# Performance work log

Measured on AMD Instinct MI355X. Metric: run time of the kernel, lower is better.

## Reference

```python
import jax, jax.numpy as jnp
import numpy as np

B, T, E, H = 2, 4096, 768, 12
D = E // H  # head_dim = 64


def setup_inputs() -> dict:
    key = jax.random.key(0)
    ks = jax.random.split(key, 9)
    s = 1.0 / np.sqrt(E)
    return {
        "x": jax.random.normal(ks[0], (B, T, E), dtype=jnp.float32),
        "wq": jax.random.normal(ks[1], (E, E), dtype=jnp.float32) * s,
        "bq": jnp.zeros((E,), dtype=jnp.float32),
        "wk": jax.random.normal(ks[2], (E, E), dtype=jnp.float32) * s,
        "bk": jnp.zeros((E,), dtype=jnp.float32),
        "wv": jax.random.normal(ks[3], (E, E), dtype=jnp.float32) * s,
        "bv": jnp.zeros((E,), dtype=jnp.float32),
        "wo": jax.random.normal(ks[4], (E, E), dtype=jnp.float32) * s,
        "bo": jnp.zeros((E,), dtype=jnp.float32),
    }


def reference(x, wq, bq, wk, bk, wv, bv, wo, bo):
    # Linear projections (torch Linear: x @ W.T + b; weights here stored as (in,out))
    q = x @ wq + bq  # (B,T,E)
    k = x @ wk + bk
    v = x @ wv + bv

    def split(t):
        return t.reshape(B, T, H, D).transpose(0, 2, 1, 3)  # (B,H,T,D)

    q, k, v = split(q), split(k), split(v)
    scale = 1.0 / np.sqrt(D).astype(np.float32)
    scores = jnp.einsum("bhtd,bhsd->bhts", q, k) * scale  # (B,H,T,T)
    causal = jnp.tril(jnp.ones((T, T), dtype=bool))
    scores = jnp.where(causal, scores, -jnp.inf)
    attn = jax.nn.softmax(scores, axis=-1)
    out = jnp.einsum("bhts,bhsd->bhtd", attn, v)  # (B,H,T,D)
    out = out.transpose(0, 2, 1, 3).reshape(B, T, E)
    return out @ wo + bo
```

## Files before the change

kernel.cpp:

```cpp
#include <hip/hip_runtime.h>
#include <hip/hip_bf16.h>

#define TSEQ 4096
#define EMB 768
#define NH 12
#define DH 64
#define BT 8192
#define NROWS (24 * TSEQ)

typedef __attribute__((ext_vector_type(8))) short bf16x8;
typedef __attribute__((ext_vector_type(4))) float f32x4;

#define FENCE() asm volatile("" ::: "memory")

__device__ __forceinline__ f32x4 mfma16(bf16x8 a, bf16x8 b, f32x4 c) {
    return __builtin_amdgcn_mfma_f32_16x16x32_bf16(a, b, c, 0, 0, 0);
}

__device__ __forceinline__ void gload16(const void* g, void* l) {
    __builtin_amdgcn_global_load_lds((const __attribute__((address_space(1))) void*)g,
                                     (__attribute__((address_space(3))) void*)l, 16, 0, 0);
}

__device__ __forceinline__ float bf2f(unsigned short u) {
    return __uint_as_float(((unsigned)u) << 16);
}

__global__ __launch_bounds__(256) void conv_all_k(const float* __restrict__ x,
                                                  __hip_bfloat16* __restrict__ xb,
                                                  const float* w0, const float* w1,
                                                  const float* w2, const float* w3,
                                                  __hip_bfloat16* o0, __hip_bfloat16* o1,
                                                  __hip_bfloat16* o2, __hip_bfloat16* o3) {
    __shared__ float tile[32][33];
    int bid = blockIdx.x;
    if (bid < 6144) {
        int i = (bid * 256 + threadIdx.x) * 4;
        float4 v = *(const float4*)(x + i);
        union { unsigned short u[4]; uint2 p; } o;
        __hip_bfloat16 t0 = __float2bfloat16(v.x); o.u[0] = *(unsigned short*)&t0;
        __hip_bfloat16 t1 = __float2bfloat16(v.y); o.u[1] = *(unsigned short*)&t1;
        __hip_bfloat16 t2 = __float2bfloat16(v.z); o.u[2] = *(unsigned short*)&t2;
        __hip_bfloat16 t3 = __float2bfloat16(v.w); o.u[3] = *(unsigned short*)&t3;
        *(uint2*)(xb + i) = o.p;
        return;
    }
    bid -= 6144;
    const int z = bid / 576, rr = bid % 576, by = rr / 24, bx = rr % 24;
    const float* w; __hip_bfloat16* o;
    switch (z) {
        case 0: w = w0; o = o0; break;
        case 1: w = w1; o = o1; break;
        case 2: w = w2; o = o2; break;
        default: w = w3; o = o3; break;
    }
    int tx = threadIdx.x & 31, ty = threadIdx.x >> 5;
    int kb = by * 32, nb = bx * 32;
    for (int i = 0; i < 32; i += 8)
        tile[ty + i][tx] = w[(size_t)(kb + ty + i) * EMB + nb + tx];
    __syncthreads();
    for (int i = 0; i < 32; i += 8)
        o[(size_t)(nb + ty + i) * EMB + kb + tx] = __float2bfloat16(tile[tx][ty + i]);
}

__device__ __forceinline__ void gemm_body(const __hip_bfloat16* __restrict__ A,
                                          const __hip_bfloat16* __restrict__ Wt,
                                          const float* __restrict__ bias,
                                          void* __restrict__ outp, int mode, float scale) {
    __shared__ alignas(16) char As[2][8192];
    __shared__ alignas(16) char Bs[2][8192];
    const int m0 = blockIdx.x * 128, n0 = blockIdx.y * 128;
    const int tid = threadIdx.x;
    const int lane = tid & 63, l15 = lane & 15, lg = lane >> 4;
    const int wave = tid >> 6, wm = wave >> 1, wn = wave & 1;
    const int swz = (l15 & 7) << 4;

    int mrow_[2]; int kelem_[2];
#pragma unroll
    for (int c = 0; c < 2; ++c) {
        int p = c * 4096 + tid * 16;
        int lrow = p >> 7, w = p & 127;
        int wp = w ^ ((lrow & 7) << 4);
        mrow_[c] = lrow + ((wp >> 6) & 1) * 64;
        kelem_[c] = (wp & 63) >> 1;
    }

    f32x4 acc[4][4];
    for (int i = 0; i < 4; ++i)
        for (int j = 0; j < 4; ++j) acc[i][j] = (f32x4){0.f, 0.f, 0.f, 0.f};

    auto stage = [&](int buf, int k0) {
#pragma unroll
        for (int c = 0; c < 2; ++c)
            gload16(A + (size_t)(m0 + mrow_[c]) * EMB + k0 + kelem_[c],
                    As[buf] + c * 4096 + wave * 1024);
#pragma unroll
        for (int c = 0; c < 2; ++c)
            gload16(Wt + (size_t)(n0 + mrow_[c]) * EMB + k0 + kelem_[c],
                    Bs[buf] + c * 4096 + wave * 1024);
    };

    stage(0, 0);
    const int NK = EMB / 32;
    for (int ks = 0; ks < NK; ++ks) {
        const int cur = ks & 1;
        asm volatile("s_waitcnt vmcnt(0)" ::: "memory");
        FENCE(); __builtin_amdgcn_s_barrier(); FENCE();
        if (ks + 1 < NK) stage(cur ^ 1, (ks + 1) * 32);
        bf16x8 af[4], bfv[4];
#pragma unroll
        for (int f = 0; f < 4; ++f)
            af[f] = *(const bf16x8*)(As[cur] + (f * 16 + l15) * 128 + ((wm * 64 + lg * 16) ^ swz));
#pragma unroll
        for (int f = 0; f < 4; ++f)
            bfv[f] = *(const bf16x8*)(Bs[cur] + (f * 16 + l15) * 128 + ((wn * 64 + lg * 16) ^ swz));
        __builtin_amdgcn_s_setprio(1);
#pragma unroll
        for (int i = 0; i < 4; ++i)
#pragma unroll
            for (int j = 0; j < 4; ++j)
                acc[i][j] = mfma16(af[i], bfv[j], acc[i][j]);
        __builtin_amdgcn_s_setprio(0);
    }

#pragma unroll
    for (int i = 0; i < 4; ++i) {
#pragma unroll
        for (int j = 0; j < 4; ++j) {
            const int n = n0 + wn * 64 + j * 16 + l15;
            const float bv = bias[n];
            const int mbase = m0 + wm * 64 + i * 16 + lg * 4;
#pragma unroll
            for (int r = 0; r < 4; ++r) {
                const int m = mbase + r;
                const float val = (acc[i][j][r] + bv) * scale;
                if (mode == 2) {
                    ((float*)outp)[(size_t)m * EMB + n] = val;
                } else {
                    const int b = m >> 12, t = m & (TSEQ - 1);
                    const int h = n >> 6, d = n & 63;
                    size_t addr;
                    if (mode == 0) addr = ((size_t)(b * NH + h) * TSEQ + t) * DH + d;
                    else           addr = ((size_t)(b * NH + h) * DH + d) * TSEQ + t;
                    ((__hip_bfloat16*)outp)[addr] = __float2bfloat16(val);
                }
            }
        }
    }
}

__global__ __launch_bounds__(256) void qkv_k(const __hip_bfloat16* __restrict__ xb,
                                             const __hip_bfloat16* __restrict__ wqT,
                                             const __hip_bfloat16* __restrict__ wkT,
                                             const __hip_bfloat16* __restrict__ wvT,
                                             const float* __restrict__ bq,
                                             const float* __restrict__ bk,
                                             const float* __restrict__ bv,
                                             __hip_bfloat16* __restrict__ qo,
                                             __hip_bfloat16* __restrict__ ko,
                                             __hip_bfloat16* __restrict__ vo) {
    const __hip_bfloat16* Wt; const float* bias; void* o; int mode; float scale;
    const float cq = 0.125f * 1.44269504089f;
    switch (blockIdx.z) {
        case 0:  Wt = wqT; bias = bq; o = qo; mode = 0; scale = cq;  break;
        case 1:  Wt = wkT; bias = bk; o = ko; mode = 0; scale = 1.f; break;
        default: Wt = wvT; bias = bv; o = vo; mode = 1; scale = 1.f; break;
    }
    gemm_body(xb, Wt, bias, o, mode, scale);
}

__global__ __launch_bounds__(256) void oprojc_k(const __hip_bfloat16* __restrict__ opart,
                                                const float* __restrict__ lpart,
                                                const __hip_bfloat16* __restrict__ Wt,
                                                const float* __restrict__ bias,
                                                float* __restrict__ out) {
    __shared__ alignas(16) char As[2][4096];
    __shared__ alignas(16) char Bs[2][8192];
    const int m0 = blockIdx.x * 64, n0 = blockIdx.y * 128;
    const int tid = threadIdx.x;
    const int lane = tid & 63, l15 = lane & 15, lg = lane >> 4;
    const int wave = tid >> 6, wm = wave >> 1, wn = wave & 1;
    const int swz = (l15 & 7) << 4;

    int amrow, akelem;
    {
        int p = tid * 16;
        int lrow = p >> 7, w = p & 127;
        int wp = w ^ ((lrow & 7) << 4);
        amrow = lrow + ((wp >> 6) & 1) * 32;
        akelem = (wp & 63) >> 1;
    }
    const int m = m0 + amrow;
    const int b_ = m >> 12, t = m & (TSEQ - 1);
    int bnrow[2], bkelem[2];
#pragma unroll
    for (int c = 0; c < 2; ++c) {
        int p = c * 4096 + tid * 16;
        int lrow = p >> 7, w = p & 127;
        int wp = w ^ ((lrow & 7) << 4);
        bnrow[c] = lrow + ((wp >> 6) & 1) * 64;
        bkelem[c] = (wp & 63) >> 1;
    }

    f32x4 acc[2][4];
    for (int i = 0; i < 2; ++i)
        for (int j = 0; j < 4; ++j) acc[i][j] = (f32x4){0.f, 0.f, 0.f, 0.f};

    auto stage = [&](int buf, int k0) {
        const int h = k0 >> 6;
        const int d0 = (k0 & 63) + akelem;
        const size_t orow = ((size_t)(b_ * NH + h)) * TSEQ + t;
        bf16x8 a0 = *(const bf16x8*)(opart + orow * DH + d0);
        bf16x8 a1 = *(const bf16x8*)(opart + ((size_t)NROWS + orow) * DH + d0);
        const float li = 1.0f / (lpart[orow] + lpart[NROWS + orow]);
        union { unsigned w[4]; uint4 v; } pk;
#pragma unroll
        for (int jp = 0; jp < 4; ++jp) {
            const float e0 = (bf2f((unsigned short)a0[2 * jp]) + bf2f((unsigned short)a1[2 * jp])) * li;
            const float e1 = (bf2f((unsigned short)a0[2 * jp + 1]) + bf2f((unsigned short)a1[2 * jp + 1])) * li;
            asm("v_cvt_pk_bf16_f32 %0, %1, %2" : "=v"(pk.w[jp]) : "v"(e0), "v"(e1));
        }
        *(uint4*)(As[buf] + wave * 1024 + lane * 16) = pk.v;
#pragma unroll
        for (int c = 0; c < 2; ++c)
            gload16(Wt + (size_t)(n0 + bnrow[c]) * EMB + k0 + bkelem[c],
                    Bs[buf] + c * 4096 + wave * 1024);
    };

    stage(0, 0);
    const int NK = EMB / 32;
    for (int ks = 0; ks < NK; ++ks) {
        const int cur = ks & 1;
        asm volatile("s_waitcnt vmcnt(0) lgkmcnt(0)" ::: "memory");
        FENCE(); __builtin_amdgcn_s_barrier(); FENCE();
        if (ks + 1 < NK) stage(cur ^ 1, (ks + 1) * 32);
        bf16x8 af[2], bfv[4];
#pragma unroll
        for (int f = 0; f < 2; ++f)
            af[f] = *(const bf16x8*)(As[cur] + (f * 16 + l15) * 128 + ((wm * 64 + lg * 16) ^ swz));
#pragma unroll
        for (int f = 0; f < 4; ++f)
            bfv[f] = *(const bf16x8*)(Bs[cur] + (f * 16 + l15) * 128 + ((wn * 64 + lg * 16) ^ swz));
        __builtin_amdgcn_s_setprio(1);
#pragma unroll
        for (int i = 0; i < 2; ++i)
#pragma unroll
            for (int j = 0; j < 4; ++j)
                acc[i][j] = mfma16(af[i], bfv[j], acc[i][j]);
        __builtin_amdgcn_s_setprio(0);
    }

#pragma unroll
    for (int i = 0; i < 2; ++i) {
#pragma unroll
        for (int j = 0; j < 4; ++j) {
            const int n = n0 + wn * 64 + j * 16 + l15;
            const float bv = bias[n];
            const int mbase = m0 + wm * 32 + i * 16 + lg * 4;
#pragma unroll
            for (int r = 0; r < 4; ++r)
                out[(size_t)(mbase + r) * EMB + n] = acc[i][j][r] + bv;
        }
    }
}

__global__ __launch_bounds__(256, 3) void attn_k(const __hip_bfloat16* __restrict__ qb,
                                                 const __hip_bfloat16* __restrict__ kb,
                                                 const __hip_bfloat16* __restrict__ vt,
                                                 __hip_bfloat16* __restrict__ opart,
                                                 float* __restrict__ lpart) {
    __shared__ alignas(16) char Ks[8192];
    __shared__ alignas(16) char Vs[8192];
    __shared__ alignas(16) char pbuf[4][4096];
    const int lane = threadIdx.x & 63, l15 = lane & 15, lg = lane >> 4;
    const int wave = threadIdx.x >> 6;
    const int bid = blockIdx.x;
    const int xcd = bid & 7, slot = bid >> 3;
    const int pair = slot & 31;
    const int parity = (slot >> 5) & 1;
    const int hgrp = slot >> 6;
    const int bh = xcd + hgrp * 8;
    const __hip_bfloat16* Qh = qb + (size_t)bh * TSEQ * DH;
    const __hip_bfloat16* Kh = kb + (size_t)bh * TSEQ * DH;
    const __hip_bfloat16* Vh = vt + (size_t)bh * DH * TSEQ;
    char* Pb = pbuf[wave];
    const int swz = (l15 & 7) << 4;
    const float M0 = 12.0f;

    bf16x8 ones8;
#pragma unroll
    for (int j = 0; j < 8; ++j) ones8[j] = (short)0x3F80;

    unsigned ka[8];
#pragma unroll
    for (int st = 0; st < 4; ++st)
#pragma unroll
        for (int ks = 0; ks < 2; ++ks)
            ka[st * 2 + ks] = (unsigned)((st * 16 + l15) * 128 + ((ks * 64 + lg * 16) ^ swz));
    char* pwh[4]; char* prh[2]; char* pwl[4]; char* prl[2];
#pragma unroll
    for (int st = 0; st < 4; ++st) {
        pwh[st] = Pb + l15 * 128 + ((st * 32 + lg * 8) ^ swz);
        pwl[st] = pwh[st] + 2048;
    }
#pragma unroll
    for (int ks = 0; ks < 2; ++ks) {
        prh[ks] = Pb + l15 * 128 + ((ks * 64 + lg * 16) ^ swz);
        prl[ks] = prh[ks] + 2048;
    }
    const int dthr = wave * 16 + l15 - lg * 4;

    int r_[2], wp_[2];
#pragma unroll
    for (int c = 0; c < 2; ++c) {
        int p = c * 4096 + wave * 1024 + lane * 16;
        int r = p >> 7, w = p & 127;
        r_[c] = r;
        wp_[c] = (w ^ ((r & 7) << 4)) >> 1;
    }

    const int lo = pair, hi = 63 - pair;
    const int q0l = lo * 64 + wave * 16;
    const int q0h = hi * 64 + wave * 16;
    const int nsb = hi + 1;

    bf16x8 qh0 = *(const bf16x8*)(Qh + (size_t)(q0h + l15) * DH + lg * 8);
    bf16x8 qh1 = *(const bf16x8*)(Qh + (size_t)(q0h + l15) * DH + 32 + lg * 8);
    bf16x8 ql0 = *(const bf16x8*)(Qh + (size_t)(q0l + l15) * DH + lg * 8);
    bf16x8 ql1 = *(const bf16x8*)(Qh + (size_t)(q0l + l15) * DH + 32 + lg * 8);

    f32x4 oh[4], ol[4];
#pragma unroll
    for (int dt = 0; dt < 4; ++dt) { oh[dt] = (f32x4){0.f,0.f,0.f,0.f}; ol[dt] = (f32x4){0.f,0.f,0.f,0.f}; }
    f32x4 lh = (f32x4){0.f,0.f,0.f,0.f}, ll = (f32x4){0.f,0.f,0.f,0.f};

    const char* kg0 = (const char*)(Kh + (size_t)r_[0] * DH + wp_[0]) + parity * 8192;
    const char* kg1 = (const char*)(Kh + (size_t)r_[1] * DH + wp_[1]) + parity * 8192;
    const char* vg0 = (const char*)(Vh + (size_t)r_[0] * TSEQ + wp_[0]) + parity * 128;
    const char* vg1 = (const char*)(Vh + (size_t)r_[1] * TSEQ + wp_[1]) + parity * 128;

#define STAGE() do {                                                             \
    gload16(kg0, Ks + wave * 1024);                                              \
    gload16(kg1, Ks + 4096 + wave * 1024);                                       \
    gload16(vg0, Vs + wave * 1024);                                              \
    gload16(vg1, Vs + 4096 + wave * 1024);                                       \
    kg0 += 16384; kg1 += 16384; vg0 += 256; vg1 += 256;                          \
} while (0)

#define QKSM(KF, Q0, Q1, MASKB, PW) do {                                         \
    f32x4 sa[4];                                                                 \
    __builtin_amdgcn_s_setprio(1);                                               \
    _Pragma("unroll")                                                            \
    for (int st = 0; st < 4; ++st) {                                             \
        f32x4 z = (f32x4){0.f, 0.f, 0.f, 0.f};                                   \
        z = mfma16(KF[st * 2 + 0], Q0, z);                                       \
        z = mfma16(KF[st * 2 + 1], Q1, z);                                       \
        sa[st] = z;                                                              \
    }                                                                            \
    __builtin_amdgcn_s_setprio(0);                                               \
    if (MASKB) {                                                                 \
        _Pragma("unroll")                                                        \
        for (int st = 0; st < 4; ++st)                                           \
            _Pragma("unroll")                                                    \
            for (int r = 0; r < 4; ++r)                                          \
                if (st * 16 + r > dthr) sa[st][r] = -INFINITY;                   \
    }                                                                            \
    _Pragma("unroll")                                                            \
    for (int st = 0; st < 4; ++st) {                                             \
        const float e0 = exp2f(sa[st][0] - M0);                                  \
        const float e1 = exp2f(sa[st][1] - M0);                                  \
        const float e2 = exp2f(sa[st][2] - M0);                                  \
        const float e3 = exp2f(sa[st][3] - M0);                                  \
        uint2 pkv;                                                               \
        asm("v_cvt_pk_bf16_f32 %0, %1, %2" : "=v"(pkv.x) : "v"(e0), "v"(e1));    \
        asm("v_cvt_pk_bf16_f32 %0, %1, %2" : "=v"(pkv.y) : "v"(e2), "v"(e3));    \
        *(uint2*)PW[st] = pkv;                                                   \
    }                                                                            \
} while (0)

#define PVU(VF, OV, LA, PR) do {                                                 \
    bf16x8 pf0 = *(const bf16x8*)PR[0];                                          \
    bf16x8 pf1 = *(const bf16x8*)PR[1];                                          \
    __builtin_amdgcn_s_setprio(1);                                               \
    LA = mfma16(pf0, ones8, LA);                                                 \
    LA = mfma16(pf1, ones8, LA);                                                 \
    _Pragma("unroll")                                                            \
    for (int dt = 0; dt < 4; ++dt)                                               \
        OV[dt] = mfma16(pf0, VF[dt * 2 + 0], OV[dt]);                            \
    _Pragma("unroll")                                                            \
    for (int dt = 0; dt < 4; ++dt)                                               \
        OV[dt] = mfma16(pf1, VF[dt * 2 + 1], OV[dt]);                            \
    __builtin_amdgcn_s_setprio(0);                                               \
} while (0)

    STAGE();
    for (int sb = parity; sb < nsb; sb += 2) {
        const bool loact = (sb <= lo);
        asm volatile("s_waitcnt vmcnt(0)" ::: "memory");
        FENCE(); __builtin_amdgcn_s_barrier(); FENCE();
        bf16x8 kf[8];
#pragma unroll
        for (int i = 0; i < 8; ++i) kf[i] = *(const bf16x8*)(Ks + ka[i]);
        QKSM(kf, qh0, qh1, (sb == hi), pwh);
        if (loact) QKSM(kf, ql0, ql1, (sb == lo), pwl);
        bf16x8 vf[8];
#pragma unroll
        for (int i = 0; i < 8; ++i) vf[i] = *(const bf16x8*)(Vs + ka[i]);
        asm volatile("s_waitcnt lgkmcnt(0)" ::: "memory");
        FENCE(); __builtin_amdgcn_s_barrier(); FENCE();
        if (sb + 2 < nsb) STAGE();
        PVU(vf, oh, lh, prh);
        if (loact) PVU(vf, ol, ll, prl);
    }

#undef PVU
#undef QKSM
#undef STAGE

    const size_t prow = ((size_t)parity * 24 + bh) * TSEQ;
    {
#pragma unroll
        for (int r = 0; r < 4; ++r) {
            const size_t base = (prow + q0h + lg * 4 + r) * DH;
#pragma unroll
            for (int dt = 0; dt < 4; ++dt)
                opart[base + dt * 16 + l15] = __float2bfloat16(oh[dt][r]);
        }
        if (l15 == 0) {
#pragma unroll
            for (int r = 0; r < 4; ++r) lpart[prow + q0h + lg * 4 + r] = lh[r];
        }
    }
    {
#pragma unroll
        for (int r = 0; r < 4; ++r) {
            const size_t base = (prow + q0l + lg * 4 + r) * DH;
#pragma unroll
            for (int dt = 0; dt < 4; ++dt)
                opart[base + dt * 16 + l15] = __float2bfloat16(ol[dt][r]);
        }
        if (l15 == 0) {
#pragma unroll
            for (int r = 0; r < 4; ++r) lpart[prow + q0l + lg * 4 + r] = ll[r];
        }
    }
}

extern "C" void kernel_launch(void* const* d_in, const int* in_sizes, int n_in,
                              void* d_out, int out_size, void* d_ws, size_t ws_size,
                              hipStream_t stream) {
    (void)in_sizes; (void)n_in; (void)out_size; (void)ws_size;
    const float* x  = (const float*)d_in[0];
    const float* wq = (const float*)d_in[1];
    const float* bq = (const float*)d_in[2];
    const float* wk = (const float*)d_in[3];
    const float* bk = (const float*)d_in[4];
    const float* wv = (const float*)d_in[5];
    const float* bv = (const float*)d_in[6];
    const float* wo = (const float*)d_in[7];
    const float* bo = (const float*)d_in[8];
    float* out = (float*)d_out;

    char* ws = (char*)d_ws;
    size_t off = 0;
    auto alloc = [&](size_t bytes) {
        char* p = ws + off;
        off += (bytes + 255) & ~(size_t)255;
        return p;
    };
    __hip_bfloat16* xb   = (__hip_bfloat16*)alloc((size_t)BT * EMB * 2);
    __hip_bfloat16* qbf  = (__hip_bfloat16*)alloc((size_t)BT * EMB * 2);
    __hip_bfloat16* kbf  = (__hip_bfloat16*)alloc((size_t)BT * EMB * 2);
    __hip_bfloat16* vtb  = (__hip_bfloat16*)alloc((size_t)BT * EMB * 2);
    __hip_bfloat16* wqT  = (__hip_bfloat16*)alloc((size_t)EMB * EMB * 2);
    __hip_bfloat16* wkT  = (__hip_bfloat16*)alloc((size_t)EMB * EMB * 2);
    __hip_bfloat16* wvT  = (__hip_bfloat16*)alloc((size_t)EMB * EMB * 2);
    __hip_bfloat16* woT  = (__hip_bfloat16*)alloc((size_t)EMB * EMB * 2);
    __hip_bfloat16* opart = (__hip_bfloat16*)alloc((size_t)2 * NROWS * DH * 2);
    float*          lpart = (float*)alloc((size_t)2 * NROWS * 4);

    conv_all_k<<<6144 + 2304, 256, 0, stream>>>(x, xb, wq, wk, wv, wo, wqT, wkT, wvT, woT);
    qkv_k<<<dim3(64, 6, 3), 256, 0, stream>>>(xb, wqT, wkT, wvT, bq, bk, bv, qbf, kbf, vtb);
    attn_k<<<1536, 256, 0, stream>>>(qbf, kbf, vtb, opart, lpart);
    oprojc_k<<<dim3(128, 6), 256, 0, stream>>>(opart, lpart, woT, bo, out);
}
```

Before: 183.7 us.

## Split hi/lo query tiles across separate waves in 512-thread attention blocks

The attention kernel now uses 8 waves per block instead of 4. Waves 0-3 handle the high query tile and waves 4-7 the low tile, where before each wave processed both tiles in sequence. Each thread stages half as many K/V loads, and each wave's P buffer shrinks to 2KB. This is meant to raise parallelism and cut per-wave register pressure. The cost is that the low-tile waves sit idle, only hitting barriers, once past their causal limit, and there are more waves per block to synchronise.

```diff
diff --git a/kernel.cpp b/kernel.cpp
--- a/kernel.cpp
+++ b/kernel.cpp
@@ -264,16 +264,19 @@
     }
 }
 
-__global__ __launch_bounds__(256, 3) void attn_k(const __hip_bfloat16* __restrict__ qb,
+__global__ __launch_bounds__(512, 4) void attn_k(const __hip_bfloat16* __restrict__ qb,
                                                  const __hip_bfloat16* __restrict__ kb,
                                                  const __hip_bfloat16* __restrict__ vt,
                                                  __hip_bfloat16* __restrict__ opart,
                                                  float* __restrict__ lpart) {
     __shared__ alignas(16) char Ks[8192];
     __shared__ alignas(16) char Vs[8192];
-    __shared__ alignas(16) char pbuf[4][4096];
-    const int lane = threadIdx.x & 63, l15 = lane & 15, lg = lane >> 4;
-    const int wave = threadIdx.x >> 6;
+    __shared__ alignas(16) char pbuf[8][2048];
+    const int tid = threadIdx.x;
+    const int lane = tid & 63, l15 = lane & 15, lg = lane >> 4;
+    const int wave = tid >> 6;
+    const int w4 = wave & 3;
+    const bool hirole = (wave < 4);
     const int bid = blockIdx.x;
     const int xcd = bid & 7, slot = bid >> 3;
     const int pair = slot & 31;
@@ -297,64 +300,51 @@
 #pragma unroll
         for (int ks = 0; ks < 2; ++ks)
             ka[st * 2 + ks] = (unsigned)((st * 16 + l15) * 128 + ((ks * 64 + lg * 16) ^ swz));
-    char* pwh[4]; char* prh[2]; char* pwl[4]; char* prl[2];
-#pragma unroll
-    for (int st = 0; st < 4; ++st) {
-        pwh[st] = Pb + l15 * 128 + ((st * 32 + lg * 8) ^ swz);
-        pwl[st] = pwh[st] + 2048;
-    }
-#pragma unroll
-    for (int ks = 0; ks < 2; ++ks) {
-        prh[ks] = Pb + l15 * 128 + ((ks * 64 + lg * 16) ^ swz);
-        prl[ks] = prh[ks] + 2048;
-    }
-    const int dthr = wave * 16 + l15 - lg * 4;
-
-    int r_[2], wp_[2];
-#pragma unroll
-    for (int c = 0; c < 2; ++c) {
-        int p = c * 4096 + wave * 1024 + lane * 16;
+    char* pw[4]; char* pr[2];
+#pragma unroll
+    for (int st = 0; st < 4; ++st) pw[st] = Pb + l15 * 128 + ((st * 32 + lg * 8) ^ swz);
+#pragma unroll
+    for (int ks = 0; ks < 2; ++ks) pr[ks] = Pb + l15 * 128 + ((ks * 64 + lg * 16) ^ swz);
+    const int dthr = w4 * 16 + l15 - lg * 4;
+
+    int r_, wp_;
+    {
+        int p = tid * 16;
         int r = p >> 7, w = p & 127;
-        r_[c] = r;
-        wp_[c] = (w ^ ((r & 7) << 4)) >> 1;
+        r_ = r;
+        wp_ = (w ^ ((r & 7) << 4)) >> 1;
     }
 
     const int lo = pair, hi = 63 - pair;
-    const int q0l = lo * 64 + wave * 16;
-    const int q0h = hi * 64 + wave * 16;
+    const int mytile = hirole ? hi : lo;
+    const int q0 = mytile * 64 + w4 * 16;
     const int nsb = hi + 1;
 
-    bf16x8 qh0 = *(const bf16x8*)(Qh + (size_t)(q0h + l15) * DH + lg * 8);
-    bf16x8 qh1 = *(const bf16x8*)(Qh + (size_t)(q0h + l15) * DH + 32 + lg * 8);
-    bf16x8 ql0 = *(const bf16x8*)(Qh + (size_t)(q0l + l15) * DH + lg * 8);
-    bf16x8 ql1 = *(const bf16x8*)(Qh + (size_t)(q0l + l15) * DH + 32 + lg * 8);
-
-    f32x4 oh[4], ol[4];
-#pragma unroll
-    for (int dt = 0; dt < 4; ++dt) { oh[dt] = (f32x4){0.f,0.f,0.f,0.f}; ol[dt] = (f32x4){0.f,0.f,0.f,0.f}; }
-    f32x4 lh = (f32x4){0.f,0.f,0.f,0.f}, ll = (f32x4){0.f,0.f,0.f,0.f};
-
-    const char* kg0 = (const char*)(Kh + (size_t)r_[0] * DH + wp_[0]) + parity * 8192;
-    const char* kg1 = (const char*)(Kh + (size_t)r_[1] * DH + wp_[1]) + parity * 8192;
-    const char* vg0 = (const char*)(Vh + (size_t)r_[0] * TSEQ + wp_[0]) + parity * 128;
-    const char* vg1 = (const char*)(Vh + (size_t)r_[1] * TSEQ + wp_[1]) + parity * 128;
+    bf16x8 q0f = *(const bf16x8*)(Qh + (size_t)(q0 + l15) * DH + lg * 8);
+    bf16x8 q1f = *(const bf16x8*)(Qh + (size_t)(q0 + l15) * DH + 32 + lg * 8);
+
+    f32x4 ov[4];
+#pragma unroll
+    for (int dt = 0; dt < 4; ++dt) ov[dt] = (f32x4){0.f, 0.f, 0.f, 0.f};
+    f32x4 la = (f32x4){0.f, 0.f, 0.f, 0.f};
+
+    const char* kg = (const char*)(Kh + (size_t)r_ * DH + wp_) + parity * 8192;
+    const char* vg = (const char*)(Vh + (size_t)r_ * TSEQ + wp_) + parity * 128;
 
 #define STAGE() do {                                                             \
-    gload16(kg0, Ks + wave * 1024);                                              \
-    gload16(kg1, Ks + 4096 + wave * 1024);                                       \
-    gload16(vg0, Vs + wave * 1024);                                              \
-    gload16(vg1, Vs + 4096 + wave * 1024);                                       \
-    kg0 += 16384; kg1 += 16384; vg0 += 256; vg1 += 256;                          \
+    gload16(kg, Ks + wave * 1024);                                               \
+    gload16(vg, Vs + wave * 1024);                                               \
+    kg += 16384; vg += 256;                                                      \
 } while (0)
 
-#define QKSM(KF, Q0, Q1, MASKB, PW) do {                                         \
+#define QKSM(KF, MASKB) do {                                                     \
     f32x4 sa[4];                                                                 \
     __builtin_amdgcn_s_setprio(1);                                               \
     _Pragma("unroll")                                                            \
     for (int st = 0; st < 4; ++st) {                                             \
         f32x4 z = (f32x4){0.f, 0.f, 0.f, 0.f};                                   \
-        z = mfma16(KF[st * 2 + 0], Q0, z);                                       \
-        z = mfma16(KF[st * 2 + 1], Q1, z);                                       \
+        z = mfma16(KF[st * 2 + 0], q0f, z);                                      \
+        z = mfma16(KF[st * 2 + 1], q1f, z);                                      \
         sa[st] = z;                                                              \
     }                                                                            \
     __builtin_amdgcn_s_setprio(0);                                               \
@@ -374,43 +364,47 @@
         uint2 pkv;                                                               \
         asm("v_cvt_pk_bf16_f32 %0, %1, %2" : "=v"(pkv.x) : "v"(e0), "v"(e1));    \
         asm("v_cvt_pk_bf16_f32 %0, %1, %2" : "=v"(pkv.y) : "v"(e2), "v"(e3));    \
-        *(uint2*)PW[st] = pkv;                                                   \
+        *(uint2*)pw[st] = pkv;                                                   \
     }                                                                            \
 } while (0)
 
-#define PVU(VF, OV, LA, PR) do {                                                 \
-    bf16x8 pf0 = *(const bf16x8*)PR[0];                                          \
-    bf16x8 pf1 = *(const bf16x8*)PR[1];                                          \
+#define PVU(VF) do {                                                             \
+    bf16x8 pf0 = *(const bf16x8*)pr[0];                                          \
+    bf16x8 pf1 = *(const bf16x8*)pr[1];                                          \
     __builtin_amdgcn_s_setprio(1);                                               \
-    LA = mfma16(pf0, ones8, LA);                                                 \
-    LA = mfma16(pf1, ones8, LA);                                                 \
+    la = mfma16(pf0, ones8, la);                                                 \
+    la = mfma16(pf1, ones8, la);                                                 \
     _Pragma("unroll")                                                            \
     for (int dt = 0; dt < 4; ++dt)                                               \
-        OV[dt] = mfma16(pf0, VF[dt * 2 + 0], OV[dt]);                            \
+        ov[dt] = mfma16(pf0, VF[dt * 2 + 0], ov[dt]);                            \
     _Pragma("unroll")                                                            \
     for (int dt = 0; dt < 4; ++dt)                                               \
-        OV[dt] = mfma16(pf1, VF[dt * 2 + 1], OV[dt]);                            \
+        ov[dt] = mfma16(pf1, VF[dt * 2 + 1], ov[dt]);                            \
     __builtin_amdgcn_s_setprio(0);                                               \
 } while (0)
 
     STAGE();
     for (int sb = parity; sb < nsb; sb += 2) {
-        const bool loact = (sb <= lo);
+        const bool act = hirole || (sb <= lo);
+        const bool maskb = hirole ? (sb == hi) : (sb == lo);
         asm volatile("s_waitcnt vmcnt(0)" ::: "memory");
         FENCE(); __builtin_amdgcn_s_barrier(); FENCE();
-        bf16x8 kf[8];
-#pragma unroll
-        for (int i = 0; i < 8; ++i) kf[i] = *(const bf16x8*)(Ks + ka[i]);
-        QKSM(kf, qh0, qh1, (sb == hi), pwh);
-        if (loact) QKSM(kf, ql0, ql1, (sb == lo), pwl);
-        bf16x8 vf[8];
-#pragma unroll
-        for (int i = 0; i < 8; ++i) vf[i] = *(const bf16x8*)(Vs + ka[i]);
-        asm volatile("s_waitcnt lgkmcnt(0)" ::: "memory");
-        FENCE(); __builtin_amdgcn_s_barrier(); FENCE();
-        if (sb + 2 < nsb) STAGE();
-        PVU(vf, oh, lh, prh);
-        if (loact) PVU(vf, ol, ll, prl);
+        if (act) {
+            bf16x8 kf[8];
+#pragma unroll
+            for (int i = 0; i < 8; ++i) kf[i] = *(const bf16x8*)(Ks + ka[i]);
+            QKSM(kf, maskb);
+            bf16x8 vf[8];
+#pragma unroll
+            for (int i = 0; i < 8; ++i) vf[i] = *(const bf16x8*)(Vs + ka[i]);
+            asm volatile("s_waitcnt lgkmcnt(0)" ::: "memory");
+            FENCE(); __builtin_amdgcn_s_barrier(); FENCE();
+            if (sb + 2 < nsb) STAGE();
+            PVU(vf);
+        } else {
+            FENCE(); __builtin_amdgcn_s_barrier(); FENCE();
+            if (sb + 2 < nsb) STAGE();
+        }
     }
 
 #undef PVU
@@ -418,31 +412,16 @@
 #undef STAGE
 
     const size_t prow = ((size_t)parity * 24 + bh) * TSEQ;
-    {
-#pragma unroll
-        for (int r = 0; r < 4; ++r) {
-            const size_t base = (prow + q0h + lg * 4 + r) * DH;
-#pragma unroll
-            for (int dt = 0; dt < 4; ++dt)
-                opart[base + dt * 16 + l15] = __float2bfloat16(oh[dt][r]);
-        }
-        if (l15 == 0) {
-#pragma unroll
-            for (int r = 0; r < 4; ++r) lpart[prow + q0h + lg * 4 + r] = lh[r];
-        }
-    }
-    {
-#pragma unroll
-        for (int r = 0; r < 4; ++r) {
-            const size_t base = (prow + q0l + lg * 4 + r) * DH;
-#pragma unroll
-            for (int dt = 0; dt < 4; ++dt)
-                opart[base + dt * 16 + l15] = __float2bfloat16(ol[dt][r]);
-        }
-        if (l15 == 0) {
-#pragma unroll
-            for (int r = 0; r < 4; ++r) lpart[prow + q0l + lg * 4 + r] = ll[r];
-        }
+#pragma unroll
+    for (int r = 0; r < 4; ++r) {
+        const size_t base = (prow + q0 + lg * 4 + r) * DH;
+#pragma unroll
+        for (int dt = 0; dt < 4; ++dt)
+            opart[base + dt * 16 + l15] = __float2bfloat16(ov[dt][r]);
+    }
+    if (l15 == 0) {
+#pragma unroll
+        for (int r = 0; r < 4; ++r) lpart[prow + q0 + lg * 4 + r] = la[r];
     }
 }
 
@@ -481,6 +460,6 @@
 
     conv_all_k<<<6144 + 2304, 256, 0, stream>>>(x, xb, wq, wk, wv, wo, wqT, wkT, wvT, woT);
     qkv_k<<<dim3(64, 6, 3), 256, 0, stream>>>(xb, wqT, wkT, wvT, bq, bk, bv, qbf, kbf, vtb);
-    attn_k<<<1536, 256, 0, stream>>>(qbf, kbf, vtb, opart, lpart);
+    attn_k<<<1536, 512, 0, stream>>>(qbf, kbf, vtb, opart, lpart);
     oprojc_k<<<dim3(128, 6), 256, 0, stream>>>(opart, lpart, woT, bo, out);
 }
```

New measurement: 193.2 us. 5.2% more time.
